# Kernel tuning notes

Hardware: AMD Instinct MI355X
Metric: run time of the kernel (lower is better)

## Reference

```python
import jax, jax.numpy as jnp
import numpy as np
from jax.scipy.linalg import solve_triangular

JITTER = 1e-4  # matches init jitter


def kernel_ard(x1, x2, log_ls, log_sf):
    # ARD RBF kernel: sf * exp(-0.5 * || (x1 - x2) / ls ||^2)
    # x1: (b,H,N,D), x2: (b,H,M,D); log_ls: (H,D); log_sf: (H,1)
    inv_ls = jnp.exp(-log_ls)[None, :, None, :]
    a = x1 * inv_ls
    b = x2 * inv_ls
    d2 = (jnp.sum(a * a, -1)[..., :, None]
          - 2.0 * jnp.einsum('bhnd,bhmd->bhnm', a, b)
          + jnp.sum(b * b, -1)[..., None, :])
    sf = jnp.exp(log_sf)[None, :, :, None]  # (1,H,1,1)
    return sf * jnp.exp(-0.5 * d2)


def sgp_forward(x, cur_k, eps, W_qkv, log_sf, log_ls, v_ind, s_sqrt_ltri, log_s_sqrt_diag, W_O_w, W_O_b):
    B, L, hdim = x.shape
    H, vd = log_ls.shape
    M = cur_k.shape[1]
    S = eps.shape[2]

    # fc_qkv + head split (q and v_gamma interleaved per head)
    qkv = (x @ W_qkv.T).reshape(B, L, H, 2 * vd).transpose(0, 2, 1, 3)  # (B,H,L,2vd)
    q, v_gamma = qkv[..., :vd], qkv[..., vd:]

    # inducing keys: first hdim rows of fc_qkv weight applied to cur_k
    W_qk = W_qkv[:hdim].reshape(H, vd, hdim)
    k_beta = jnp.einsum('hdk,mk->hmd', W_qk, cur_k[0])[None]  # (1,H,M,vd)
    k_beta_b = jnp.broadcast_to(k_beta, (B, H, M, vd))
    v_beta = jnp.transpose(v_ind, (1, 0, 2, 3))               # (1,H,M,vd)
    log_ssqrt = jnp.transpose(log_s_sqrt_diag, (1, 0, 2, 3))  # (1,H,vd,M)

    K_qq = kernel_ard(q, q, log_ls, log_sf)               # (B,H,L,L)
    K_qk_beta = kernel_ard(q, k_beta_b, log_ls, log_sf)   # (B,H,L,M)
    K_kk = kernel_ard(k_beta, k_beta, log_ls, log_sf)     # (1,H,M,M)
    K_kq = jnp.swapaxes(K_qk_beta, -1, -2)                # (B,H,M,L)

    eyeM = jnp.eye(M, dtype=x.dtype)
    s_sqrt = jnp.exp(log_ssqrt)
    # diag_embed(s_sqrt) + strictly-lower-tri part of s_sqrt_ltri
    s_local = eyeM * s_sqrt[..., :, None] + jnp.tril(jnp.transpose(s_sqrt_ltri, (1, 0, 2, 3, 4)), -1)  # (1,H,vd,M,M)

    chol = jnp.linalg.cholesky(K_kk + JITTER * eyeM)      # (1,H,M,M)
    cholB = jnp.broadcast_to(chol, (B, H, M, M))
    v1 = solve_triangular(cholB, K_kq, lower=True)        # (B,H,M,L)
    v2 = solve_triangular(cholB, K_kq @ v_gamma, lower=True)  # (B,H,M,vd)
    v3 = jnp.einsum('bhml,hdmn->bhdln', v1, s_local[0])   # (B,H,vd,L,M)

    mean1 = K_qq @ v_gamma                                # (B,H,L,vd)
    mean = mean1 - jnp.einsum('bhml,bhmd->bhld', v1, v2) + K_qk_beta @ v_beta

    covar1 = jnp.diagonal(K_qq, axis1=-2, axis2=-1)[:, :, None, :, None]  # (B,H,1,L,1)
    v3sq = jnp.swapaxes(jnp.sum(v3 * v3, -1), 2, 3)[:, :, None]           # (B,H,1,L,vd)
    v1sq = jnp.sum(v1 * v1, 2)[:, :, None, :, None]                       # (B,H,1,L,1)
    chol_covar = jnp.sqrt(covar1 + v3sq - v1sq)           # (B,H,1,L,vd)

    samples = mean[:, :, None] + chol_covar * eps         # (B,H,S,L,vd)
    samples = samples.transpose(0, 2, 3, 1, 4).reshape(B, S, L, H * vd)
    out = samples @ W_O_w.T + W_O_b                       # (B,S,L,hdim); dropout p=0 -> identity

    # KL divergence (training path)
    kl = jnp.asarray(-0.5 * M * vd * H, dtype=x.dtype)
    kl = kl + 0.5 * jnp.sum(s_local * s_local)
    kl = kl + 0.5 * jnp.einsum('ohmd,ohmn,ohnd->', v_beta, K_kk, v_beta)
    per_b = jnp.sum(v_gamma * mean1, axis=(1, 2, 3)) - jnp.sum(v2 * v2, axis=(1, 2, 3))
    kl = kl + 0.5 * jnp.mean(per_b)
    kl = kl - jnp.sum(log_ssqrt)
    return out, kl


def setup_inputs():
    key = jax.random.key(0)
    ks = jax.random.split(key, 10)
    B, L, H, vd, M, S = 8, 512, 8, 64, 64, 2
    hdim = H * vd
    return {
        "x": jax.random.normal(ks[0], (B, L, hdim), jnp.float32),
        "cur_k": jax.random.normal(ks[1], (1, M, hdim), jnp.float32),
        "eps": jax.random.normal(ks[2], (B, H, S, L, vd), jnp.float32),
        "W_qkv": jax.random.normal(ks[3], (2 * hdim, hdim), jnp.float32) / np.float32(np.sqrt(hdim)),
        "log_sf": jnp.zeros((H, 1), jnp.float32),
        "log_ls": jax.random.normal(ks[4], (H, vd), jnp.float32),
        "v_ind": jax.random.normal(ks[5], (H, 1, M, vd), jnp.float32),
        "s_sqrt_ltri": 0.1 * jax.random.normal(ks[6], (H, 1, vd, M, M), jnp.float32),
        "log_s_sqrt_diag": jax.random.normal(ks[7], (H, 1, vd, M), jnp.float32),
        "W_O_w": jax.random.normal(ks[8], (hdim, hdim), jnp.float32) / np.float32(np.sqrt(hdim)),
        "W_O_b": jax.random.normal(ks[9], (hdim,), jnp.float32),
    }


def reference(x, cur_k, eps, W_qkv, log_sf, log_ls, v_ind, s_sqrt_ltri, log_s_sqrt_diag, W_O_w, W_O_b):
    return sgp_forward(x, cur_k, eps, W_qkv, log_sf, log_ls, v_ind, s_sqrt_ltri, log_s_sqrt_diag, W_O_w, W_O_b)
```

## Files before the change

kernel.cpp:

```cpp
#include <hip/hip_runtime.h>
#include <math.h>


#define NB 8
#define NL 512
#define NH 8
#define NVD 64
#define NM 64
#define NS 2

static const size_t OFF_QS   = 0;
static const size_t OFF_VG   = OFF_QS   + 2097152;
static const size_t OFF_QN   = OFF_VG   + 2097152;
static const size_t OFF_KBS  = OFF_QN   + 32768;
static const size_t OFF_KBN  = OFF_KBS  + 32768;
static const size_t OFF_LINV = OFF_KBN  + 512;
static const size_t OFF_V1   = OFF_LINV + 32768;
static const size_t OFF_V1SQ = OFF_V1   + 2097152;
static const size_t OFF_MEAN = OFF_V1SQ + 32768;
static const size_t OFF_V2   = OFF_MEAN + 2097152;
static const size_t OFF_SBUF = OFF_V2   + 262144;
static const size_t OFF_V3   = OFF_SBUF + 2097152;
static const size_t OFF_SMP  = OFF_V3   + 2097152;
static const size_t OFF_KL   = OFF_SMP  + 4194304;

__device__ __forceinline__ void load_tile_t(float* dst, const float* src, int ld) {
  int t = threadIdx.x;
  int r = t >> 2;
  int c0 = (t & 3) * 16;
#pragma unroll
  for (int q = 0; q < 4; ++q) {
    float4 v = *(const float4*)(src + (size_t)r * ld + c0 + q * 4);
    int c = c0 + q * 4;
    dst[(c + 0) * 68 + r] = v.x;
    dst[(c + 1) * 68 + r] = v.y;
    dst[(c + 2) * 68 + r] = v.z;
    dst[(c + 3) * 68 + r] = v.w;
  }
}
__device__ __forceinline__ void load_tile_n(float* dst, const float* src, int ld) {
  int t = threadIdx.x;
  int r = t >> 2;
  int c0 = (t & 3) * 16;
#pragma unroll
  for (int q = 0; q < 4; ++q) {
    float4 v = *(const float4*)(src + (size_t)r * ld + c0 + q * 4);
    *(float4*)(dst + r * 68 + c0 + q * 4) = v;
  }
}
__device__ __forceinline__ void mma64(const float* aT, const float* bT, int tr, int tn,
                                      float acc[4][4]) {
#pragma unroll 16
  for (int k = 0; k < 64; ++k) {
    float4 av = *(const float4*)(aT + k * 68 + tr);
    float4 bv = *(const float4*)(bT + k * 68 + tn);
    float a[4] = {av.x, av.y, av.z, av.w};
    float b[4] = {bv.x, bv.y, bv.z, bv.w};
#pragma unroll
    for (int i = 0; i < 4; ++i)
#pragma unroll
      for (int j = 0; j < 4; ++j) acc[i][j] = fmaf(a[i], b[j], acc[i][j]);
  }
}
__device__ __forceinline__ void mma64_dual(const float* aT, const float* b1T,
                                           const float* b2T, int tr, int tn,
                                           float acc1[4][4], float acc2[4][4]) {
#pragma unroll 8
  for (int k = 0; k < 64; ++k) {
    float4 av = *(const float4*)(aT + k * 68 + tr);
    float4 b1 = *(const float4*)(b1T + k * 68 + tn);
    float4 b2 = *(const float4*)(b2T + k * 68 + tn);
    float a[4] = {av.x, av.y, av.z, av.w};
    float p[4] = {b1.x, b1.y, b1.z, b1.w};
    float q[4] = {b2.x, b2.y, b2.z, b2.w};
#pragma unroll
    for (int i = 0; i < 4; ++i)
#pragma unroll
      for (int j = 0; j < 4; ++j) {
        acc1[i][j] = fmaf(a[i], p[j], acc1[i][j]);
        acc2[i][j] = fmaf(a[i], q[j], acc2[i][j]);
      }
  }
}

template <int EPI>
__global__ __launch_bounds__(256) void gemm_nt_kernel(
    const float* __restrict__ A, const float* __restrict__ Bm, int K,
    float* __restrict__ o0, float* __restrict__ o1, const float* __restrict__ aux,
    float* __restrict__ qn) {
  __shared__ float As[16][68];
  __shared__ float Bs[16][68];
  const int t = threadIdx.x;
  const int r0 = blockIdx.x * 64;
  const int n0 = blockIdx.y * 64;
  const int lr = t >> 2;
  const int lk = (t & 3) * 4;
  const int tr = (t >> 4) * 4;
  const int tn = (t & 15) * 4;
  const float* Ap = A + (size_t)(r0 + lr) * K + lk;
  const float* Bp = Bm + (size_t)(n0 + lr) * K + lk;
  float acc[4][4] = {};
  for (int k0 = 0; k0 < K; k0 += 16) {
    float4 a4 = *(const float4*)(Ap + k0);
    float4 b4 = *(const float4*)(Bp + k0);
    As[lk + 0][lr] = a4.x; As[lk + 1][lr] = a4.y; As[lk + 2][lr] = a4.z; As[lk + 3][lr] = a4.w;
    Bs[lk + 0][lr] = b4.x; Bs[lk + 1][lr] = b4.y; Bs[lk + 2][lr] = b4.z; Bs[lk + 3][lr] = b4.w;
    __syncthreads();
#pragma unroll
    for (int k = 0; k < 16; ++k) {
      float4 av = *(const float4*)&As[k][tr];
      float4 bv = *(const float4*)&Bs[k][tn];
      float a[4] = {av.x, av.y, av.z, av.w};
      float b[4] = {bv.x, bv.y, bv.z, bv.w};
#pragma unroll
      for (int i = 0; i < 4; ++i)
#pragma unroll
        for (int j = 0; j < 4; ++j) acc[i][j] = fmaf(a[i], b[j], acc[i][j]);
    }
    __syncthreads();
  }
  if (EPI == 0) {
    const int h = n0 >> 7;
    const bool isq = (n0 & 64) == 0;
    if (isq) {
      float invls[4];
#pragma unroll
      for (int j = 0; j < 4; ++j) invls[j] = __expf(-aux[h * 64 + tn + j]);
      float* red = &As[0][0];
#pragma unroll
      for (int i = 0; i < 4; ++i) {
        int r = r0 + tr + i;
        int b = r >> 9, l = r & 511;
        float4 o;
        o.x = acc[i][0] * invls[0];
        o.y = acc[i][1] * invls[1];
        o.z = acc[i][2] * invls[2];
        o.w = acc[i][3] * invls[3];
        *(float4*)(o0 + (((size_t)(b * 8 + h)) * 512 + l) * 64 + tn) = o;
        red[(tr + i) * 17 + (t & 15)] = o.x * o.x + o.y * o.y + o.z * o.z + o.w * o.w;
      }
      __syncthreads();
      if (t < 64) {
        float s = 0.f;
#pragma unroll
        for (int g = 0; g < 16; ++g) s += red[t * 17 + g];
        int r = r0 + t;
        int b = r >> 9, l = r & 511;
        qn[(b * 8 + h) * 512 + l] = s;
      }
    } else {
#pragma unroll
      for (int i = 0; i < 4; ++i) {
        int r = r0 + tr + i;
        int b = r >> 9, l = r & 511;
        float4 o = {acc[i][0], acc[i][1], acc[i][2], acc[i][3]};
        *(float4*)(o1 + (((size_t)(b * 8 + h)) * 512 + l) * 64 + tn) = o;
      }
    }
  } else {
#pragma unroll
    for (int i = 0; i < 4; ++i) {
      int r = r0 + tr + i;
      float4 o;
      o.x = acc[i][0] + aux[n0 + tn + 0];
      o.y = acc[i][1] + aux[n0 + tn + 1];
      o.z = acc[i][2] + aux[n0 + tn + 2];
      o.w = acc[i][3] + aux[n0 + tn + 3];
      *(float4*)(o0 + (size_t)r * 512 + n0 + tn) = o;
    }
  }
}

__global__ __launch_bounds__(256) void k2_kbeta(const float* __restrict__ W,
                                                const float* __restrict__ ckg,
                                                const float* __restrict__ log_ls,
                                                float* __restrict__ kbs,
                                                float* __restrict__ kbn) {
  __shared__ float ck[512];
  __shared__ float kb[64];
  int h = blockIdx.x >> 6, m = blockIdx.x & 63;
  int t = threadIdx.x;
  ck[t] = ckg[m * 512 + t];
  ck[t + 256] = ckg[m * 512 + t + 256];
  __syncthreads();
  int w = t >> 6, lane = t & 63;
  for (int d = w; d < 64; d += 4) {
    const float* row = W + (size_t)(h * 64 + d) * 512;
    float p = 0.f;
    for (int k = lane; k < 512; k += 64) p = fmaf(row[k], ck[k], p);
#pragma unroll
    for (int off = 32; off > 0; off >>= 1) p += __shfl_down(p, off);
    if (lane == 0) {
      float v = p * __expf(-log_ls[h * 64 + d]);
      kbs[(size_t)h * 4096 + m * 64 + d] = v;
      kb[d] = v;
    }
  }
  __syncthreads();
  if (w == 0) {
    float v = kb[lane];
    v *= v;
#pragma unroll
    for (int off = 32; off > 0; off >>= 1) v += __shfl_down(v, off);
    if (lane == 0) kbn[h * 64 + m] = v;
  }
}

__global__ __launch_bounds__(64) void k3_chol(const float* __restrict__ kbs,
                                              const float* __restrict__ kbn,
                                              const float* __restrict__ vind,
                                              const float* __restrict__ log_sf,
                                              float* __restrict__ linv_g,
                                              float* __restrict__ klbuf) {
  __shared__ float Am[64][65];
  __shared__ float Bm[64][65];
  __shared__ float kn[64];
  int h = blockIdx.x;
  int t = threadIdx.x;
  for (int m = 0; m < 64; ++m) Bm[m][t] = kbs[(size_t)h * 4096 + m * 64 + t];
  kn[t] = kbn[h * 64 + t];
  float lsf = log_sf[h];
  __syncthreads();
  float nh = -0.5f * kn[t] + lsf;
  for (int n = 0; n < 64; ++n) {
    float dt = 0.f;
#pragma unroll 8
    for (int d = 0; d < 64; ++d) dt = fmaf(Bm[t][d], Bm[n][d], dt);
    Am[t][n] = __expf(dt + nh - 0.5f * kn[n]);
  }
  __syncthreads();
  for (int m = 0; m < 64; ++m) Bm[m][t] = vind[(size_t)h * 4096 + m * 64 + t];
  __syncthreads();
  float s = 0.f;
  for (int m = 0; m < 64; ++m) {
    float tt = 0.f;
    for (int n = 0; n < 64; ++n) tt = fmaf(Am[m][n], Bm[n][t], tt);
    s = fmaf(Bm[m][t], tt, s);
  }
#pragma unroll
  for (int off = 32; off > 0; off >>= 1) s += __shfl_down(s, off);
  if (t == 0) atomicAdd(&klbuf[1], 0.5f * s);
  __syncthreads();
  Am[t][t] += 1e-4f;
  __syncthreads();
  for (int k = 0; k < 64; ++k) {
    if (t == k) Am[k][k] = sqrtf(Am[k][k]);
    __syncthreads();
    if (t > k) Am[t][k] /= Am[k][k];
    __syncthreads();
    if (t > k) {
      float f = Am[t][k];
      for (int j = k + 1; j <= t; ++j) Am[t][j] = fmaf(-f, Am[j][k], Am[t][j]);
    }
    __syncthreads();
  }
  for (int i = 0; i < t; ++i) Bm[i][t] = 0.f;
  Bm[t][t] = 1.f / Am[t][t];
  for (int i = t + 1; i < 64; ++i) {
    float a = 0.f;
    for (int j = t; j < i; ++j) a = fmaf(Am[i][j], Bm[j][t], a);
    Bm[i][t] = -a / Am[i][i];
  }
  __syncthreads();
  for (int m = 0; m < 64; ++m) linv_g[(size_t)h * 4096 + m * 64 + t] = Bm[m][t];
}

__global__ __launch_bounds__(256) void ks_build(const float* __restrict__ ltri,
                                                const float* __restrict__ ldiag,
                                                float* __restrict__ sbuf,
                                                float* __restrict__ klbuf) {
  __shared__ float r1[256], r2[256];
  int hd = blockIdx.x;
  int t = threadIdx.x;
  float p2 = 0.f, pl = 0.f;
  for (int i = t; i < 4096; i += 256) {
    int m = i >> 6, n = i & 63;
    float v;
    if (m == n) v = __expf(ldiag[hd * 64 + m]);
    else if (m > n) v = ltri[(size_t)hd * 4096 + i];
    else v = 0.f;
    sbuf[(size_t)hd * 4096 + i] = v;
    p2 = fmaf(0.5f * v, v, p2);
  }
  if (t < 64) pl = ldiag[hd * 64 + t];
  r1[t] = p2;
  r2[t] = pl;
  __syncthreads();
  for (int sft = 128; sft > 0; sft >>= 1) {
    if (t < sft) { r1[t] += r1[t + sft]; r2[t] += r2[t + sft]; }
    __syncthreads();
  }
  if (t == 0) {
    atomicAdd(&klbuf[0], r1[0]);
    atomicAdd(&klbuf[2], r2[0]);
  }
}

__global__ __launch_bounds__(256) void k4_fused(
    const float* __restrict__ qs, const float* __restrict__ qn,
    const float* __restrict__ kbs, const float* __restrict__ kbn,
    const float* __restrict__ linv, const float* __restrict__ vind,
    const float* __restrict__ log_sf, float* __restrict__ v1,
    float* __restrict__ v1sq, float* __restrict__ meanbuf) {
  extern __shared__ float lds[];
  float* qsT = lds;
  float* kbT = lds + 4352;
  float* liT = lds + 2 * 4352;
  float* vbN = lds + 3 * 4352;
  float* red = lds + 4 * 4352;
  __shared__ float qn_s[64], kbn_s[64];
  const int lt = blockIdx.x, bh = blockIdx.y;
  const int h = bh & 7;
  const int t = threadIdx.x;
  const int l0 = lt * 64;
  const int tr = (t >> 4) * 4, tn = (t & 15) * 4;
  load_tile_t(qsT, qs + ((size_t)bh * 512 + l0) * 64, 64);
  load_tile_t(kbT, kbs + (size_t)h * 4096, 64);
  load_tile_t(liT, linv + (size_t)h * 4096, 64);
  load_tile_n(vbN, vind + (size_t)h * 4096, 64);
  if (t < 64) {
    qn_s[t] = qn[bh * 512 + l0 + t];
    kbn_s[t] = kbn[h * 64 + t];
  }
  __syncthreads();
  float acc[4][4] = {};
  mma64(qsT, kbT, tr, tn, acc);
  const float lsf = log_sf[h];
  float arow[4], acol[4];
#pragma unroll
  for (int i = 0; i < 4; ++i) arow[i] = -0.5f * qn_s[tr + i];
#pragma unroll
  for (int j = 0; j < 4; ++j) acol[j] = -0.5f * kbn_s[tn + j] + lsf;
  float kv[4][4];
#pragma unroll
  for (int i = 0; i < 4; ++i)
#pragma unroll
    for (int j = 0; j < 4; ++j) kv[i][j] = __expf(acc[i][j] + arow[i] + acol[j]);
  __syncthreads();
#pragma unroll
  for (int i = 0; i < 4; ++i)
#pragma unroll
    for (int j = 0; j < 4; ++j) qsT[(tn + j) * 68 + (tr + i)] = kv[i][j];
  __syncthreads();
  float a2[4][4] = {};
  float a3[4][4] = {};
  mma64_dual(qsT, liT, vbN, tr, tn, a2, a3);
#pragma unroll
  for (int i = 0; i < 4; ++i) {
    float4 o = {a2[i][0], a2[i][1], a2[i][2], a2[i][3]};
    *(float4*)(v1 + ((size_t)bh * 512 + l0 + tr + i) * 64 + tn) = o;
    red[(tr + i) * 17 + (t & 15)] =
        a2[i][0] * a2[i][0] + a2[i][1] * a2[i][1] + a2[i][2] * a2[i][2] + a2[i][3] * a2[i][3];
    float4 o3 = {a3[i][0], a3[i][1], a3[i][2], a3[i][3]};
    *(float4*)(meanbuf + ((size_t)bh * 512 + l0 + tr + i) * 64 + tn) = o3;
  }
  __syncthreads();
  if (t < 64) {
    float s2 = 0.f;
#pragma unroll
    for (int g = 0; g < 16; ++g) s2 += red[t * 17 + g];
    v1sq[bh * 512 + l0 + t] = s2;
  }
}

__global__ __launch_bounds__(256) void k5_v2(const float* __restrict__ v1,
                                             const float* __restrict__ vg,
                                             float* __restrict__ v2,
                                             float* __restrict__ klbuf) {
  __shared__ float v1t[64 * 68];
  __shared__ float vgt[64 * 68];
  __shared__ float redp[256];
  const int bh = blockIdx.x;
  const int b = bh >> 3;
  const int t = threadIdx.x;
  const int tr = (t >> 4) * 4, tn = (t & 15) * 4;
  float acc[4][4] = {};
  for (int c0 = 0; c0 < 512; c0 += 64) {
    __syncthreads();
    load_tile_n(v1t, v1 + ((size_t)bh * 512 + c0) * 64, 64);
    load_tile_n(vgt, vg + ((size_t)bh * 512 + c0) * 64, 64);
    __syncthreads();
    mma64(v1t, vgt, tr, tn, acc);
  }
  float p = 0.f;
#pragma unroll
  for (int i = 0; i < 4; ++i) {
    float4 o = {acc[i][0], acc[i][1], acc[i][2], acc[i][3]};
    *(float4*)(v2 + ((size_t)bh * 64 + tr + i) * 64 + tn) = o;
    p += acc[i][0] * acc[i][0] + acc[i][1] * acc[i][1] + acc[i][2] * acc[i][2] +
         acc[i][3] * acc[i][3];
  }
  redp[t] = p;
  __syncthreads();
  if (t < 64) {
    float s = redp[t] + redp[t + 64] + redp[t + 128] + redp[t + 192];
#pragma unroll
    for (int off = 32; off > 0; off >>= 1) s += __shfl_down(s, off);
    if (t == 0) atomicAdd(&klbuf[11 + b], s);
  }
}

__global__ __launch_bounds__(256) void k6_mean1(const float* __restrict__ qs,
                                                const float* __restrict__ qn,
                                                const float* __restrict__ vg,
                                                const float* __restrict__ log_sf,
                                                float* __restrict__ meanbuf,
                                                float* __restrict__ klbuf) {
  extern __shared__ float lds[];
  float* qrT = lds;
  float* qcT = lds + 4352;
  float* sT = lds + 2 * 4352;
  float* vgN = lds + 3 * 4352;
  __shared__ float qn_r[64], qn_c[64], redp[256];
  const int lt = blockIdx.x, bh = blockIdx.y;
  const int b = bh >> 3, h = bh & 7;
  const int l0 = lt * 64;
  const int t = threadIdx.x;
  const int tr = (t >> 4) * 4, tn = (t & 15) * 4;
  load_tile_t(qrT, qs + ((size_t)bh * 512 + l0) * 64, 64);
  if (t < 64) qn_r[t] = qn[bh * 512 + l0 + t];
  const float lsf = log_sf[h];
  float acc[4][4] = {};
  for (int c0 = 0; c0 < 512; c0 += 64) {
    __syncthreads();
    load_tile_t(qcT, qs + ((size_t)bh * 512 + c0) * 64, 64);
    load_tile_n(vgN, vg + ((size_t)bh * 512 + c0) * 64, 64);
    if (t < 64) qn_c[t] = qn[bh * 512 + c0 + t];
    __syncthreads();
    float dt[4][4] = {};
    mma64(qrT, qcT, tr, tn, dt);
    float arow[4], acol[4];
#pragma unroll
    for (int i = 0; i < 4; ++i) arow[i] = -0.5f * qn_r[tr + i];
#pragma unroll
    for (int j = 0; j < 4; ++j) acol[j] = -0.5f * qn_c[tn + j] + lsf;
#pragma unroll
    for (int i = 0; i < 4; ++i)
#pragma unroll
      for (int j = 0; j < 4; ++j)
        sT[(tn + j) * 68 + (tr + i)] = __expf(dt[i][j] + arow[i] + acol[j]);
    __syncthreads();
    mma64(sT, vgN, tr, tn, acc);
  }
  float pb = 0.f;
#pragma unroll
  for (int i = 0; i < 4; ++i) {
    size_t rowbase = ((size_t)bh * 512 + l0 + tr + i) * 64 + tn;
    float4 vgr = *(const float4*)(vg + rowbase);
    float4 mb = *(const float4*)(meanbuf + rowbase);
    pb += acc[i][0] * vgr.x + acc[i][1] * vgr.y + acc[i][2] * vgr.z + acc[i][3] * vgr.w;
    mb.x += acc[i][0]; mb.y += acc[i][1]; mb.z += acc[i][2]; mb.w += acc[i][3];
    *(float4*)(meanbuf + rowbase) = mb;
  }
  redp[t] = pb;
  __syncthreads();
  if (t < 64) {
    float s = redp[t] + redp[t + 64] + redp[t + 128] + redp[t + 192];
#pragma unroll
    for (int off = 32; off > 0; off >>= 1) s += __shfl_down(s, off);
    if (t == 0) atomicAdd(&klbuf[3 + b], s);
  }
}

__global__ __launch_bounds__(256) void k10_v3sq(const float* __restrict__ v1,
                                                const float* __restrict__ sbuf,
                                                float* __restrict__ v3) {
  __shared__ float v1T[64 * 68];
  __shared__ float sN[64 * 68];
  __shared__ float red[64 * 17];
  const int x = blockIdx.x;
  const int lt = blockIdx.y;
  const int bh = x >> 6;
  const int hd = (bh & 7) * 64 + (x & 63);
  const int t = threadIdx.x;
  const int tr = (t & 15) * 4;
  const int tn = (t >> 4) * 4;
  const int kstart = (t >> 6) << 4;
  load_tile_t(v1T, v1 + ((size_t)bh * 512 + lt * 64) * 64, 64);
  load_tile_n(sN, sbuf + (size_t)hd * 4096, 64);
  __syncthreads();
  float acc[4][4] = {};
  for (int k0 = kstart; k0 < 64; k0 += 16) {
#pragma unroll
    for (int kk = 0; kk < 16; ++kk) {
      const int k = k0 + kk;
      float4 av = *(const float4*)(v1T + k * 68 + tr);
      float4 bv = *(const float4*)(sN + k * 68 + tn);
      float a[4] = {av.x, av.y, av.z, av.w};
      float b[4] = {bv.x, bv.y, bv.z, bv.w};
#pragma unroll
      for (int i = 0; i < 4; ++i)
#pragma unroll
        for (int j = 0; j < 4; ++j) acc[i][j] = fmaf(a[i], b[j], acc[i][j]);
    }
  }
#pragma unroll
  for (int i = 0; i < 4; ++i)
    red[(tr + i) * 17 + (t >> 4)] =
        acc[i][0] * acc[i][0] + acc[i][1] * acc[i][1] + acc[i][2] * acc[i][2] +
        acc[i][3] * acc[i][3];
  __syncthreads();
  if (t < 64) {
    float s = 0.f;
#pragma unroll
    for (int g = 0; g < 16; ++g) s += red[t * 17 + g];
    v3[(size_t)x * 512 + lt * 64 + t] = s;
  }
}

__global__ __launch_bounds__(256) void k8_samples(
    const float* __restrict__ v1, const float* __restrict__ v2,
    const float* __restrict__ meanbuf, const float* __restrict__ v3,
    const float* __restrict__ v1sq, const float* __restrict__ eps,
    const float* __restrict__ log_sf, float* __restrict__ smp) {
  extern __shared__ float lds[];
  float* v1T = lds;
  float* v2N = lds + 4352;
  float* v3T = lds + 2 * 4352;
  __shared__ float v1sq_s[64];
  const int lt = blockIdx.x, bh = blockIdx.y;
  const int b = bh >> 3, h = bh & 7;
  const int l0 = lt * 64;
  const int t = threadIdx.x;
  const int tr = (t >> 4) * 4, tn = (t & 15) * 4;
  load_tile_t(v1T, v1 + ((size_t)bh * 512 + l0) * 64, 64);
  load_tile_n(v2N, v2 + (size_t)bh * 4096, 64);
  load_tile_n(v3T, v3 + (size_t)bh * 64 * 512 + l0, 512);
  if (t < 64) v1sq_s[t] = v1sq[bh * 512 + l0 + t];
  __syncthreads();
  float acc[4][4] = {};
  mma64(v1T, v2N, tr, tn, acc);
  const float sf = __expf(log_sf[h]);
#pragma unroll
  for (int i = 0; i < 4; ++i) {
    const int l = l0 + tr + i;
    size_t mbase = ((size_t)bh * 512 + l) * 64 + tn;
    float4 mb = *(const float4*)(meanbuf + mbase);
    float mean[4] = {mb.x - acc[i][0], mb.y - acc[i][1], mb.z - acc[i][2], mb.w - acc[i][3]};
    float cc[4];
#pragma unroll
    for (int j = 0; j < 4; ++j) {
      float var = sf + v3T[(tn + j) * 68 + (tr + i)] - v1sq_s[tr + i];
      cc[j] = sqrtf(var);
    }
#pragma unroll
    for (int s2 = 0; s2 < 2; ++s2) {
      float4 ep = *(const float4*)(eps + (((size_t)bh * 2 + s2) * 512 + l) * 64 + tn);
      float4 o;
      o.x = mean[0] + cc[0] * ep.x;
      o.y = mean[1] + cc[1] * ep.y;
      o.z = mean[2] + cc[2] * ep.z;
      o.w = mean[3] + cc[3] * ep.w;
      *(float4*)(smp + (((size_t)(b * 2 + s2) * 512 + l) * 512) + h * 64 + tn) = o;
    }
  }
}

__global__ void kfin(const float* __restrict__ klbuf, float* __restrict__ dout) {
  if (threadIdx.x == 0 && blockIdx.x == 0) {
    double pb = 0.0;
    for (int b = 0; b < 8; ++b) pb += (double)klbuf[3 + b] - (double)klbuf[11 + b];
    double kl = -16384.0 + (double)klbuf[0] + (double)klbuf[1] - (double)klbuf[2] + pb / 16.0;
    dout[4194304] = (float)kl;
  }
}

extern "C" void kernel_launch(void* const* d_in, const int* in_sizes, int n_in,
                              void* d_out, int out_size, void* d_ws, size_t ws_size,
                              hipStream_t stream) {
  (void)in_sizes; (void)n_in; (void)out_size; (void)ws_size;
  const float* x     = (const float*)d_in[0];
  const float* cur_k = (const float*)d_in[1];
  const float* eps   = (const float*)d_in[2];
  const float* W_qkv = (const float*)d_in[3];
  const float* lsf   = (const float*)d_in[4];
  const float* lls   = (const float*)d_in[5];
  const float* vind  = (const float*)d_in[6];
  const float* ltri  = (const float*)d_in[7];
  const float* ldia  = (const float*)d_in[8];
  const float* Wo    = (const float*)d_in[9];
  const float* Wob   = (const float*)d_in[10];
  float* out = (float*)d_out;
  float* ws = (float*)d_ws;
  float* qs   = ws + OFF_QS;
  float* vg   = ws + OFF_VG;
  float* qn   = ws + OFF_QN;
  float* kbs  = ws + OFF_KBS;
  float* kbn  = ws + OFF_KBN;
  float* linv = ws + OFF_LINV;
  float* v1   = ws + OFF_V1;
  float* v1s  = ws + OFF_V1SQ;
  float* mean = ws + OFF_MEAN;
  float* v2   = ws + OFF_V2;
  float* sb   = ws + OFF_SBUF;
  float* v3   = ws + OFF_V3;
  float* smp  = ws + OFF_SMP;
  float* kl   = ws + OFF_KL;

  hipMemsetAsync(kl, 0, 32 * sizeof(float), stream);
  gemm_nt_kernel<0><<<dim3(64, 16), 256, 0, stream>>>(x, W_qkv, 512, qs, vg, lls, qn);
  k2_kbeta<<<512, 256, 0, stream>>>(W_qkv, cur_k, lls, kbs, kbn);
  k3_chol<<<8, 64, 0, stream>>>(kbs, kbn, vind, lsf, linv, kl);
  ks_build<<<512, 256, 0, stream>>>(ltri, ldia, sb, kl);
  k4_fused<<<dim3(8, 64), 256, 73984, stream>>>(qs, qn, kbs, kbn, linv, vind, lsf, v1, v1s, mean);
  k5_v2<<<64, 256, 0, stream>>>(v1, vg, v2, kl);
  k6_mean1<<<dim3(8, 64), 256, 69632, stream>>>(qs, qn, vg, lsf, mean, kl);
  k10_v3sq<<<dim3(4096, 8), 256, 0, stream>>>(v1, sb, v3);
  k8_samples<<<dim3(8, 64), 256, 52224, stream>>>(v1, v2, mean, v3, v1s, eps, lsf, smp);
  gemm_nt_kernel<1><<<dim3(128, 8), 256, 0, stream>>>(smp, Wo, 512, out, nullptr, Wob, nullptr);
  kfin<<<1, 64, 0, stream>>>(kl, out);
}
```

Baseline: 696.3 us.

## Use split-bf16 MFMA for v3 quadratic form and output projection GEMM

Replaces the scalar FP32 v3 kernel and the output projection GEMM with MFMA 16x16x32 bf16 kernels. To keep near-FP32 accuracy, each operand is split into high and low bf16 halves and three MFMA products are accumulated (hi*hi, hi*lo, lo*hi). Producers (k4, ks_build, k8, a new Wo conversion kernel) now emit these split bf16 copies, and the S matrix is stored transposed. The KL accumulators move to double atomics and the variance is clamped before sqrt. The cost is extra conversion work and a small risk of reduced precision.

Result: slower. 790.2 us (+13.5%).

```diff
diff --git a/kernel.cpp b/kernel.cpp
--- a/kernel.cpp
+++ b/kernel.cpp
@@ -2,12 +2,8 @@
 #include <math.h>
 
 
-#define NB 8
-#define NL 512
-#define NH 8
-#define NVD 64
-#define NM 64
-#define NS 2
+using bf16x8 = __attribute__((ext_vector_type(8))) short;
+using f32x4  = __attribute__((ext_vector_type(4))) float;
 
 static const size_t OFF_QS   = 0;
 static const size_t OFF_VG   = OFF_QS   + 2097152;
@@ -19,10 +15,27 @@
 static const size_t OFF_V1SQ = OFF_V1   + 2097152;
 static const size_t OFF_MEAN = OFF_V1SQ + 32768;
 static const size_t OFF_V2   = OFF_MEAN + 2097152;
-static const size_t OFF_SBUF = OFF_V2   + 262144;
-static const size_t OFF_V3   = OFF_SBUF + 2097152;
-static const size_t OFF_SMP  = OFF_V3   + 2097152;
-static const size_t OFF_KL   = OFF_SMP  + 4194304;
+static const size_t OFF_V1H  = OFF_V2   + 262144;
+static const size_t OFF_V1L  = OFF_V1H  + 1048576;
+static const size_t OFF_STH  = OFF_V1L  + 1048576;
+static const size_t OFF_STL  = OFF_STH  + 1048576;
+static const size_t OFF_V3   = OFF_STL  + 1048576;
+static const size_t OFF_WOH  = OFF_V3   + 2097152;
+static const size_t OFF_WOL  = OFF_WOH  + 131072;
+static const size_t OFF_KLD  = OFF_WOL  + 131072;
+
+__device__ __forceinline__ unsigned short f2bf(float x) {
+  unsigned u = __float_as_uint(x);
+  u += 0x7FFFu + ((u >> 16) & 1u);
+  return (unsigned short)(u >> 16);
+}
+__device__ __forceinline__ float bf2f(unsigned short s) {
+  return __uint_as_float(((unsigned)s) << 16);
+}
+__device__ __forceinline__ void splitbf(float x, unsigned short& h, unsigned short& l) {
+  h = f2bf(x);
+  l = f2bf(x - bf2f(h));
+}
 
 __device__ __forceinline__ void load_tile_t(float* dst, const float* src, int ld) {
   int t = threadIdx.x;
@@ -83,10 +96,9 @@
   }
 }
 
-template <int EPI>
-__global__ __launch_bounds__(256) void gemm_nt_kernel(
-    const float* __restrict__ A, const float* __restrict__ Bm, int K,
-    float* __restrict__ o0, float* __restrict__ o1, const float* __restrict__ aux,
+__global__ __launch_bounds__(256) void gemm0(
+    const float* __restrict__ A, const float* __restrict__ Bm,
+    float* __restrict__ qs, float* __restrict__ vg, const float* __restrict__ lls,
     float* __restrict__ qn) {
   __shared__ float As[16][68];
   __shared__ float Bs[16][68];
@@ -97,10 +109,10 @@
   const int lk = (t & 3) * 4;
   const int tr = (t >> 4) * 4;
   const int tn = (t & 15) * 4;
-  const float* Ap = A + (size_t)(r0 + lr) * K + lk;
-  const float* Bp = Bm + (size_t)(n0 + lr) * K + lk;
+  const float* Ap = A + (size_t)(r0 + lr) * 512 + lk;
+  const float* Bp = Bm + (size_t)(n0 + lr) * 512 + lk;
   float acc[4][4] = {};
-  for (int k0 = 0; k0 < K; k0 += 16) {
+  for (int k0 = 0; k0 < 512; k0 += 16) {
     float4 a4 = *(const float4*)(Ap + k0);
     float4 b4 = *(const float4*)(Bp + k0);
     As[lk + 0][lr] = a4.x; As[lk + 1][lr] = a4.y; As[lk + 2][lr] = a4.z; As[lk + 3][lr] = a4.w;
@@ -119,54 +131,41 @@
     }
     __syncthreads();
   }
-  if (EPI == 0) {
-    const int h = n0 >> 7;
-    const bool isq = (n0 & 64) == 0;
-    if (isq) {
-      float invls[4];
-#pragma unroll
-      for (int j = 0; j < 4; ++j) invls[j] = __expf(-aux[h * 64 + tn + j]);
-      float* red = &As[0][0];
-#pragma unroll
-      for (int i = 0; i < 4; ++i) {
-        int r = r0 + tr + i;
-        int b = r >> 9, l = r & 511;
-        float4 o;
-        o.x = acc[i][0] * invls[0];
-        o.y = acc[i][1] * invls[1];
-        o.z = acc[i][2] * invls[2];
-        o.w = acc[i][3] * invls[3];
-        *(float4*)(o0 + (((size_t)(b * 8 + h)) * 512 + l) * 64 + tn) = o;
-        red[(tr + i) * 17 + (t & 15)] = o.x * o.x + o.y * o.y + o.z * o.z + o.w * o.w;
-      }
-      __syncthreads();
-      if (t < 64) {
-        float s = 0.f;
-#pragma unroll
-        for (int g = 0; g < 16; ++g) s += red[t * 17 + g];
-        int r = r0 + t;
-        int b = r >> 9, l = r & 511;
-        qn[(b * 8 + h) * 512 + l] = s;
-      }
-    } else {
-#pragma unroll
-      for (int i = 0; i < 4; ++i) {
-        int r = r0 + tr + i;
-        int b = r >> 9, l = r & 511;
-        float4 o = {acc[i][0], acc[i][1], acc[i][2], acc[i][3]};
-        *(float4*)(o1 + (((size_t)(b * 8 + h)) * 512 + l) * 64 + tn) = o;
-      }
-    }
-  } else {
+  const int h = n0 >> 7;
+  const bool isq = (n0 & 64) == 0;
+  if (isq) {
+    float invls[4];
+#pragma unroll
+    for (int j = 0; j < 4; ++j) invls[j] = __expf(-lls[h * 64 + tn + j]);
+    float* red = &As[0][0];
 #pragma unroll
     for (int i = 0; i < 4; ++i) {
       int r = r0 + tr + i;
+      int b = r >> 9, l = r & 511;
       float4 o;
-      o.x = acc[i][0] + aux[n0 + tn + 0];
-      o.y = acc[i][1] + aux[n0 + tn + 1];
-      o.z = acc[i][2] + aux[n0 + tn + 2];
-      o.w = acc[i][3] + aux[n0 + tn + 3];
-      *(float4*)(o0 + (size_t)r * 512 + n0 + tn) = o;
+      o.x = acc[i][0] * invls[0];
+      o.y = acc[i][1] * invls[1];
+      o.z = acc[i][2] * invls[2];
+      o.w = acc[i][3] * invls[3];
+      *(float4*)(qs + (((size_t)(b * 8 + h)) * 512 + l) * 64 + tn) = o;
+      red[(tr + i) * 17 + (t & 15)] = o.x * o.x + o.y * o.y + o.z * o.z + o.w * o.w;
+    }
+    __syncthreads();
+    if (t < 64) {
+      float s = 0.f;
+#pragma unroll
+      for (int g = 0; g < 16; ++g) s += red[t * 17 + g];
+      int r = r0 + t;
+      int b = r >> 9, l = r & 511;
+      qn[(b * 8 + h) * 512 + l] = s;
+    }
+  } else {
+#pragma unroll
+    for (int i = 0; i < 4; ++i) {
+      int r = r0 + tr + i;
+      int b = r >> 9, l = r & 511;
+      float4 o = {acc[i][0], acc[i][1], acc[i][2], acc[i][3]};
+      *(float4*)(vg + (((size_t)(b * 8 + h)) * 512 + l) * 64 + tn) = o;
     }
   }
 }
@@ -211,7 +210,7 @@
                                               const float* __restrict__ vind,
                                               const float* __restrict__ log_sf,
                                               float* __restrict__ linv_g,
-                                              float* __restrict__ klbuf) {
+                                              double* __restrict__ klbuf) {
   __shared__ float Am[64][65];
   __shared__ float Bm[64][65];
   __shared__ float kn[64];
@@ -239,7 +238,7 @@
   }
 #pragma unroll
   for (int off = 32; off > 0; off >>= 1) s += __shfl_down(s, off);
-  if (t == 0) atomicAdd(&klbuf[1], 0.5f * s);
+  if (t == 0) atomicAdd(&klbuf[1], 0.5 * (double)s);
   __syncthreads();
   Am[t][t] += 1e-4f;
   __syncthreads();
@@ -267,19 +266,23 @@
 
 __global__ __launch_bounds__(256) void ks_build(const float* __restrict__ ltri,
                                                 const float* __restrict__ ldiag,
-                                                float* __restrict__ sbuf,
-                                                float* __restrict__ klbuf) {
+                                                unsigned short* __restrict__ sth,
+                                                unsigned short* __restrict__ stl,
+                                                double* __restrict__ klbuf) {
   __shared__ float r1[256], r2[256];
   int hd = blockIdx.x;
   int t = threadIdx.x;
   float p2 = 0.f, pl = 0.f;
   for (int i = t; i < 4096; i += 256) {
-    int m = i >> 6, n = i & 63;
+    int n = i >> 6, m = i & 63;
     float v;
     if (m == n) v = __expf(ldiag[hd * 64 + m]);
-    else if (m > n) v = ltri[(size_t)hd * 4096 + i];
+    else if (m > n) v = ltri[(size_t)hd * 4096 + m * 64 + n];
     else v = 0.f;
-    sbuf[(size_t)hd * 4096 + i] = v;
+    unsigned short h, l;
+    splitbf(v, h, l);
+    sth[(size_t)hd * 4096 + i] = h;
+    stl[(size_t)hd * 4096 + i] = l;
     p2 = fmaf(0.5f * v, v, p2);
   }
   if (t < 64) pl = ldiag[hd * 64 + t];
@@ -291,9 +294,20 @@
     __syncthreads();
   }
   if (t == 0) {
-    atomicAdd(&klbuf[0], r1[0]);
-    atomicAdd(&klbuf[2], r2[0]);
-  }
+    atomicAdd(&klbuf[0], (double)r1[0]);
+    atomicAdd(&klbuf[2], (double)r2[0]);
+  }
+}
+
+__global__ __launch_bounds__(256) void kconv_wo(const float* __restrict__ w,
+                                                unsigned short* __restrict__ wh,
+                                                unsigned short* __restrict__ wl) {
+  int i = blockIdx.x * 256 + threadIdx.x;
+  float v = w[i];
+  unsigned short h, l;
+  splitbf(v, h, l);
+  wh[i] = h;
+  wl[i] = l;
 }
 
 __global__ __launch_bounds__(256) void k4_fused(
@@ -301,6 +315,7 @@
     const float* __restrict__ kbs, const float* __restrict__ kbn,
     const float* __restrict__ linv, const float* __restrict__ vind,
     const float* __restrict__ log_sf, float* __restrict__ v1,
+    unsigned short* __restrict__ v1h, unsigned short* __restrict__ v1l,
     float* __restrict__ v1sq, float* __restrict__ meanbuf) {
   extern __shared__ float lds[];
   float* qsT = lds;
@@ -347,12 +362,21 @@
   mma64_dual(qsT, liT, vbN, tr, tn, a2, a3);
 #pragma unroll
   for (int i = 0; i < 4; ++i) {
+    const size_t rowbase = ((size_t)bh * 512 + l0 + tr + i) * 64 + tn;
     float4 o = {a2[i][0], a2[i][1], a2[i][2], a2[i][3]};
-    *(float4*)(v1 + ((size_t)bh * 512 + l0 + tr + i) * 64 + tn) = o;
+    *(float4*)(v1 + rowbase) = o;
+    short4 sh, sl;
+    unsigned short hh, ll;
+    splitbf(o.x, hh, ll); sh.x = (short)hh; sl.x = (short)ll;
+    splitbf(o.y, hh, ll); sh.y = (short)hh; sl.y = (short)ll;
+    splitbf(o.z, hh, ll); sh.z = (short)hh; sl.z = (short)ll;
+    splitbf(o.w, hh, ll); sh.w = (short)hh; sl.w = (short)ll;
+    *(short4*)(v1h + rowbase) = sh;
+    *(short4*)(v1l + rowbase) = sl;
     red[(tr + i) * 17 + (t & 15)] =
         a2[i][0] * a2[i][0] + a2[i][1] * a2[i][1] + a2[i][2] * a2[i][2] + a2[i][3] * a2[i][3];
     float4 o3 = {a3[i][0], a3[i][1], a3[i][2], a3[i][3]};
-    *(float4*)(meanbuf + ((size_t)bh * 512 + l0 + tr + i) * 64 + tn) = o3;
+    *(float4*)(meanbuf + rowbase) = o3;
   }
   __syncthreads();
   if (t < 64) {
@@ -366,7 +390,7 @@
 __global__ __launch_bounds__(256) void k5_v2(const float* __restrict__ v1,
                                              const float* __restrict__ vg,
                                              float* __restrict__ v2,
-                                             float* __restrict__ klbuf) {
+                                             double* __restrict__ klbuf) {
   __shared__ float v1t[64 * 68];
   __shared__ float vgt[64 * 68];
   __shared__ float redp[256];
@@ -396,7 +420,7 @@
     float s = redp[t] + redp[t + 64] + redp[t + 128] + redp[t + 192];
 #pragma unroll
     for (int off = 32; off > 0; off >>= 1) s += __shfl_down(s, off);
-    if (t == 0) atomicAdd(&klbuf[11 + b], s);
+    if (t == 0) atomicAdd(&klbuf[11 + b], (double)s);
   }
 }
 
@@ -405,7 +429,7 @@
                                                 const float* __restrict__ vg,
                                                 const float* __restrict__ log_sf,
                                                 float* __restrict__ meanbuf,
-                                                float* __restrict__ klbuf) {
+                                                double* __restrict__ klbuf) {
   extern __shared__ float lds[];
   float* qrT = lds;
   float* qcT = lds + 4352;
@@ -458,53 +482,69 @@
     float s = redp[t] + redp[t + 64] + redp[t + 128] + redp[t + 192];
 #pragma unroll
     for (int off = 32; off > 0; off >>= 1) s += __shfl_down(s, off);
-    if (t == 0) atomicAdd(&klbuf[3 + b], s);
-  }
-}
-
-__global__ __launch_bounds__(256) void k10_v3sq(const float* __restrict__ v1,
-                                                const float* __restrict__ sbuf,
+    if (t == 0) atomicAdd(&klbuf[3 + b], (double)s);
+  }
+}
+
+__global__ __launch_bounds__(256) void k10_mfma(const unsigned short* __restrict__ v1h,
+                                                const unsigned short* __restrict__ v1l,
+                                                const unsigned short* __restrict__ sth,
+                                                const unsigned short* __restrict__ stl,
                                                 float* __restrict__ v3) {
-  __shared__ float v1T[64 * 68];
-  __shared__ float sN[64 * 68];
-  __shared__ float red[64 * 17];
-  const int x = blockIdx.x;
-  const int lt = blockIdx.y;
-  const int bh = x >> 6;
-  const int hd = (bh & 7) * 64 + (x & 63);
+  const int bh = blockIdx.x;
+  const int l0 = blockIdx.y * 64;
+  const int dz = blockIdx.z;
+  const int h = bh & 7;
   const int t = threadIdx.x;
-  const int tr = (t & 15) * 4;
-  const int tn = (t >> 4) * 4;
-  const int kstart = (t >> 6) << 4;
-  load_tile_t(v1T, v1 + ((size_t)bh * 512 + lt * 64) * 64, 64);
-  load_tile_n(sN, sbuf + (size_t)hd * 4096, 64);
-  __syncthreads();
-  float acc[4][4] = {};
-  for (int k0 = kstart; k0 < 64; k0 += 16) {
-#pragma unroll
-    for (int kk = 0; kk < 16; ++kk) {
-      const int k = k0 + kk;
-      float4 av = *(const float4*)(v1T + k * 68 + tr);
-      float4 bv = *(const float4*)(sN + k * 68 + tn);
-      float a[4] = {av.x, av.y, av.z, av.w};
-      float b[4] = {bv.x, bv.y, bv.z, bv.w};
-#pragma unroll
-      for (int i = 0; i < 4; ++i)
-#pragma unroll
-        for (int j = 0; j < 4; ++j) acc[i][j] = fmaf(a[i], b[j], acc[i][j]);
-    }
-  }
-#pragma unroll
-  for (int i = 0; i < 4; ++i)
-    red[(tr + i) * 17 + (t >> 4)] =
-        acc[i][0] * acc[i][0] + acc[i][1] * acc[i][1] + acc[i][2] * acc[i][2] +
-        acc[i][3] * acc[i][3];
-  __syncthreads();
-  if (t < 64) {
-    float s = 0.f;
-#pragma unroll
-    for (int g = 0; g < 16; ++g) s += red[t * 17 + g];
-    v3[(size_t)x * 512 + lt * 64 + t] = s;
+  const int wv = t >> 6;
+  const int lane = t & 63;
+  const int lr = lane & 15;
+  const int kq = lane >> 4;
+  const size_t arow = ((size_t)bh * 512 + l0 + wv * 16 + lr) * 64;
+  bf16x8 ah[2], al[2];
+#pragma unroll
+  for (int kk = 0; kk < 2; ++kk) {
+    const int kb = kk * 32 + kq * 8;
+    ah[kk] = *(const bf16x8*)(v1h + arow + kb);
+    al[kk] = *(const bf16x8*)(v1l + arow + kb);
+  }
+  for (int dd = 0; dd < 16; ++dd) {
+    const int d = dz * 16 + dd;
+    const int hd = h * 64 + d;
+    f32x4 acc[4];
+#pragma unroll
+    for (int ns = 0; ns < 4; ++ns) acc[ns] = (f32x4){0.f, 0.f, 0.f, 0.f};
+#pragma unroll
+    for (int ns = 0; ns < 4; ++ns) {
+      const size_t scol = (size_t)hd * 4096 + (size_t)(ns * 16 + lr) * 64;
+#pragma unroll
+      for (int kk = 0; kk < 2; ++kk) {
+        const int kb = kk * 32 + kq * 8;
+        bf16x8 bh8 = *(const bf16x8*)(sth + scol + kb);
+        bf16x8 bl8 = *(const bf16x8*)(stl + scol + kb);
+        acc[ns] = __builtin_amdgcn_mfma_f32_16x16x32_bf16(ah[kk], bh8, acc[ns], 0, 0, 0);
+        acc[ns] = __builtin_amdgcn_mfma_f32_16x16x32_bf16(ah[kk], bl8, acc[ns], 0, 0, 0);
+        acc[ns] = __builtin_amdgcn_mfma_f32_16x16x32_bf16(al[kk], bh8, acc[ns], 0, 0, 0);
+      }
+    }
+    float s[4];
+#pragma unroll
+    for (int r = 0; r < 4; ++r) {
+      s[r] = acc[0][r] * acc[0][r] + acc[1][r] * acc[1][r] + acc[2][r] * acc[2][r] +
+             acc[3][r] * acc[3][r];
+    }
+#pragma unroll
+    for (int off = 1; off <= 8; off <<= 1) {
+#pragma unroll
+      for (int r = 0; r < 4; ++r) s[r] += __shfl_xor(s[r], off);
+    }
+    if (lr == 0) {
+      const size_t base = ((size_t)(bh * 64 + d)) * 512 + l0 + wv * 16 + kq * 4;
+      v3[base + 0] = s[0];
+      v3[base + 1] = s[1];
+      v3[base + 2] = s[2];
+      v3[base + 3] = s[3];
+    }
   }
 }
 
@@ -512,7 +552,8 @@
     const float* __restrict__ v1, const float* __restrict__ v2,
     const float* __restrict__ meanbuf, const float* __restrict__ v3,
     const float* __restrict__ v1sq, const float* __restrict__ eps,
-    const float* __restrict__ log_sf, float* __restrict__ smp) {
+    const float* __restrict__ log_sf, unsigned short* __restrict__ smph,
+    unsigned short* __restrict__ smpl) {
   extern __shared__ float lds[];
   float* v1T = lds;
   float* v2N = lds + 4352;
@@ -541,26 +582,77 @@
 #pragma unroll
     for (int j = 0; j < 4; ++j) {
       float var = sf + v3T[(tn + j) * 68 + (tr + i)] - v1sq_s[tr + i];
-      cc[j] = sqrtf(var);
+      cc[j] = sqrtf(fmaxf(var, 0.f));
     }
 #pragma unroll
     for (int s2 = 0; s2 < 2; ++s2) {
       float4 ep = *(const float4*)(eps + (((size_t)bh * 2 + s2) * 512 + l) * 64 + tn);
-      float4 o;
-      o.x = mean[0] + cc[0] * ep.x;
-      o.y = mean[1] + cc[1] * ep.y;
-      o.z = mean[2] + cc[2] * ep.z;
-      o.w = mean[3] + cc[3] * ep.w;
-      *(float4*)(smp + (((size_t)(b * 2 + s2) * 512 + l) * 512) + h * 64 + tn) = o;
-    }
-  }
-}
-
-__global__ void kfin(const float* __restrict__ klbuf, float* __restrict__ dout) {
+      float o[4];
+      o[0] = mean[0] + cc[0] * ep.x;
+      o[1] = mean[1] + cc[1] * ep.y;
+      o[2] = mean[2] + cc[2] * ep.z;
+      o[3] = mean[3] + cc[3] * ep.w;
+      short4 sh, sl;
+      unsigned short hh, ll;
+      splitbf(o[0], hh, ll); sh.x = (short)hh; sl.x = (short)ll;
+      splitbf(o[1], hh, ll); sh.y = (short)hh; sl.y = (short)ll;
+      splitbf(o[2], hh, ll); sh.z = (short)hh; sl.z = (short)ll;
+      splitbf(o[3], hh, ll); sh.w = (short)hh; sl.w = (short)ll;
+      const size_t obase = (((size_t)(b * 2 + s2) * 512 + l) * 512) + h * 64 + tn;
+      *(short4*)(smph + obase) = sh;
+      *(short4*)(smpl + obase) = sl;
+    }
+  }
+}
+
+__global__ __launch_bounds__(256) void gemm1_mfma(const unsigned short* __restrict__ smph,
+                                                  const unsigned short* __restrict__ smpl,
+                                                  const unsigned short* __restrict__ woh,
+                                                  const unsigned short* __restrict__ wol,
+                                                  const float* __restrict__ bias,
+                                                  float* __restrict__ out) {
+  const int r0 = blockIdx.x * 64;
+  const int n0 = blockIdx.y * 64;
+  const int t = threadIdx.x;
+  const int wv = t >> 6;
+  const int lane = t & 63;
+  const int lr = lane & 15;
+  const int kq = lane >> 4;
+  const size_t arow = ((size_t)(r0 + wv * 16 + lr)) * 512;
+  f32x4 acc[4];
+#pragma unroll
+  for (int ns = 0; ns < 4; ++ns) acc[ns] = (f32x4){0.f, 0.f, 0.f, 0.f};
+  for (int ks = 0; ks < 16; ++ks) {
+    const int kb = ks * 32 + kq * 8;
+    bf16x8 ah = *(const bf16x8*)(smph + arow + kb);
+    bf16x8 al = *(const bf16x8*)(smpl + arow + kb);
+#pragma unroll
+    for (int ns = 0; ns < 4; ++ns) {
+      const size_t brow = ((size_t)(n0 + ns * 16 + lr)) * 512 + kb;
+      bf16x8 bh8 = *(const bf16x8*)(woh + brow);
+      bf16x8 bl8 = *(const bf16x8*)(wol + brow);
+      acc[ns] = __builtin_amdgcn_mfma_f32_16x16x32_bf16(ah, bh8, acc[ns], 0, 0, 0);
+      acc[ns] = __builtin_amdgcn_mfma_f32_16x16x32_bf16(ah, bl8, acc[ns], 0, 0, 0);
+      acc[ns] = __builtin_amdgcn_mfma_f32_16x16x32_bf16(al, bh8, acc[ns], 0, 0, 0);
+    }
+  }
+#pragma unroll
+  for (int ns = 0; ns < 4; ++ns) {
+    const int outc = n0 + ns * 16 + lr;
+    const float bc = bias[outc];
+    const int rbase = r0 + wv * 16 + kq * 4;
+#pragma unroll
+    for (int r = 0; r < 4; ++r) {
+      out[(size_t)(rbase + r) * 512 + outc] = acc[ns][r] + bc;
+    }
+  }
+}
+
+__global__ void kfin(const double* __restrict__ klbuf, float* __restrict__ dout) {
   if (threadIdx.x == 0 && blockIdx.x == 0) {
     double pb = 0.0;
-    for (int b = 0; b < 8; ++b) pb += (double)klbuf[3 + b] - (double)klbuf[11 + b];
-    double kl = -16384.0 + (double)klbuf[0] + (double)klbuf[1] - (double)klbuf[2] + pb / 16.0;
+    for (int b = 0; b < 8; ++b) pb += klbuf[3 + b] - klbuf[11 + b];
+    double kl = -16384.0 + klbuf[0] + klbuf[1] - klbuf[2] + pb / 16.0;
     dout[4194304] = (float)kl;
   }
 }
@@ -592,21 +684,30 @@
   float* v1s  = ws + OFF_V1SQ;
   float* mean = ws + OFF_MEAN;
   float* v2   = ws + OFF_V2;
-  float* sb   = ws + OFF_SBUF;
   float* v3   = ws + OFF_V3;
-  float* smp  = ws + OFF_SMP;
-  float* kl   = ws + OFF_KL;
-
-  hipMemsetAsync(kl, 0, 32 * sizeof(float), stream);
-  gemm_nt_kernel<0><<<dim3(64, 16), 256, 0, stream>>>(x, W_qkv, 512, qs, vg, lls, qn);
+  unsigned short* v1h = (unsigned short*)(ws + OFF_V1H);
+  unsigned short* v1l = (unsigned short*)(ws + OFF_V1L);
+  unsigned short* sth = (unsigned short*)(ws + OFF_STH);
+  unsigned short* stl = (unsigned short*)(ws + OFF_STL);
+  unsigned short* woh = (unsigned short*)(ws + OFF_WOH);
+  unsigned short* wol = (unsigned short*)(ws + OFF_WOL);
+  unsigned short* smph = (unsigned short*)(ws + OFF_QS);
+  unsigned short* smpl = (unsigned short*)(ws + OFF_VG);
+  double* kld = (double*)(ws + OFF_KLD);
+
+  hipMemsetAsync(kld, 0, 32 * sizeof(double), stream);
+  gemm0<<<dim3(64, 16), 256, 0, stream>>>(x, W_qkv, qs, vg, lls, qn);
   k2_kbeta<<<512, 256, 0, stream>>>(W_qkv, cur_k, lls, kbs, kbn);
-  k3_chol<<<8, 64, 0, stream>>>(kbs, kbn, vind, lsf, linv, kl);
-  ks_build<<<512, 256, 0, stream>>>(ltri, ldia, sb, kl);
-  k4_fused<<<dim3(8, 64), 256, 73984, stream>>>(qs, qn, kbs, kbn, linv, vind, lsf, v1, v1s, mean);
-  k5_v2<<<64, 256, 0, stream>>>(v1, vg, v2, kl);
-  k6_mean1<<<dim3(8, 64), 256, 69632, stream>>>(qs, qn, vg, lsf, mean, kl);
-  k10_v3sq<<<dim3(4096, 8), 256, 0, stream>>>(v1, sb, v3);
-  k8_samples<<<dim3(8, 64), 256, 52224, stream>>>(v1, v2, mean, v3, v1s, eps, lsf, smp);
-  gemm_nt_kernel<1><<<dim3(128, 8), 256, 0, stream>>>(smp, Wo, 512, out, nullptr, Wob, nullptr);
-  kfin<<<1, 64, 0, stream>>>(kl, out);
-}
+  k3_chol<<<8, 64, 0, stream>>>(kbs, kbn, vind, lsf, linv, kld);
+  ks_build<<<512, 256, 0, stream>>>(ltri, ldia, sth, stl, kld);
+  kconv_wo<<<1024, 256, 0, stream>>>(Wo, woh, wol);
+  k4_fused<<<dim3(8, 64), 256, 73984, stream>>>(qs, qn, kbs, kbn, linv, vind, lsf,
+                                                v1, v1h, v1l, v1s, mean);
+  k5_v2<<<64, 256, 0, stream>>>(v1, vg, v2, kld);
+  k6_mean1<<<dim3(8, 64), 256, 69632, stream>>>(qs, qn, vg, lsf, mean, kld);
+  k10_mfma<<<dim3(64, 8, 4), 256, 0, stream>>>(v1h, v1l, sth, stl, v3);
+  k8_samples<<<dim3(8, 64), 256, 52224, stream>>>(v1, v2, mean, v3, v1s, eps, lsf,
+                                                  smph, smpl);
+  gemm1_mfma<<<dim3(128, 8), 256, 0, stream>>>(smph, smpl, woh, wol, Wob, out);
+  kfin<<<1, 64, 0, stream>>>(kld, out);
+}
```
